# Kernel tuning notes

Measured on AMD Instinct MI355X. Metric: run time of the kernel, lower is better.

The kernel has to match this reference:

```python
import jax, jax.numpy as jnp
import numpy as np
import math

B_SZ, L_SEQ, IN_DIM, D_MODEL, OUT_DIM = 8, 4096, 256, 512, 256
RMIN, RMAX = 0.8, 0.99


def setup_inputs() -> dict:
    key = jax.random.key(0)
    ks = jax.random.split(key, 9)
    inputs = jax.random.normal(ks[0], (B_SZ, L_SEQ, IN_DIM), dtype=jnp.float32)
    # A-parameterization per LRUBlock.init_A
    u1 = jax.random.uniform(ks[1], (D_MODEL,), dtype=jnp.float32)
    u2 = jax.random.uniform(ks[2], (D_MODEL,), dtype=jnp.float32)
    nu_log = jnp.log(-0.5 * jnp.log(u1 * (RMAX + RMIN) * (RMAX - RMIN) + RMIN ** 2))
    theta_log = jnp.log(2 * math.pi * u2)
    # NB: original stores gamma (not log gamma) and exponentiates it in forward; replicate.
    gamma_log = jnp.sqrt(1.0 - jnp.exp(-jnp.exp(nu_log)) ** 2)
    B_re = jax.random.uniform(ks[3], (D_MODEL, IN_DIM), dtype=jnp.float32) / math.sqrt(2 * IN_DIM)
    B_im = jax.random.uniform(ks[4], (D_MODEL, IN_DIM), dtype=jnp.float32) / math.sqrt(2 * IN_DIM)
    C_re = jax.random.uniform(ks[5], (OUT_DIM, D_MODEL), dtype=jnp.float32) / math.sqrt(D_MODEL)
    C_im = jax.random.uniform(ks[6], (OUT_DIM, D_MODEL), dtype=jnp.float32) / math.sqrt(D_MODEL)
    D = jax.random.uniform(ks[7], (OUT_DIM, IN_DIM), dtype=jnp.float32) / math.sqrt(IN_DIM)
    return {"inputs": inputs, "nu_log": nu_log, "theta_log": theta_log,
            "gamma_log": gamma_log, "B_re": B_re, "B_im": B_im,
            "C_re": C_re, "C_im": C_im, "D": D}


def reference(inputs, nu_log, theta_log, gamma_log, B_re, B_im, C_re, C_im, D):
    # skip connection: [b, l, in] x [out, in] -> [b, l, out]
    skip = jnp.einsum('blh,dh->bld', inputs, D)
    L = inputs.shape[1]
    # diagonal complex transition A = exp(-exp(nu) + i*exp(theta)), [d_model]
    A = jnp.exp(jax.lax.complex(-jnp.exp(nu_log), jnp.exp(theta_log)))
    Bc = jax.lax.complex(B_re, B_im) * jnp.exp(gamma_log)[:, None]
    # input projection u = inputs @ B^T : [b, l, d_model] complex64
    u = jnp.einsum('blh,dh->bld', inputs.astype(jnp.complex64), Bc)
    # convolution kernel H[d, t] = A[d]^t, linear conv via length-2L FFT
    H = A[:, None] ** jnp.arange(L)  # [d_model, L]
    n = 2 * L
    h_f = jnp.fft.fft(H, n=n, axis=1)          # [d_model, 2L]
    u_f = jnp.fft.fft(u, n=n, axis=1)          # [b, 2L, d_model]
    x = jnp.fft.ifft(u_f * h_f.T, axis=1)[:, :L]  # [b, L, d_model] complex64
    y = jnp.einsum('blh,nh->bln', x, jax.lax.complex(C_re, C_im)).real + skip
    return (x, y)
```

## Files before the change

kernel.cpp:

```cpp
#include <hip/hip_runtime.h>
#include <math.h>

#define B_SZ 8
#define L_SEQ 4096
#define IN_DIM 256
#define D_MODEL 512
#define OUT_DIM 256
#define M_ROWS (B_SZ*L_SEQ)
#define CH 64
#define NCH (L_SEQ/CH)

#define Y_OFF ((size_t)M_ROWS*D_MODEL)

#define XIM_B   ((size_t)0)
#define WT_B    ((size_t)33554432)
#define CDT_B   ((size_t)34078720)
#define S_B     ((size_t)34734080)

typedef __attribute__((ext_vector_type(8))) short short8;
typedef __attribute__((ext_vector_type(4))) float f32x4;
typedef unsigned short ushort_t;

__device__ __forceinline__ unsigned short f2b(float f) {
    unsigned u = __float_as_uint(f);
    unsigned r = u + 0x7FFF + ((u >> 16) & 1);
    return (unsigned short)(r >> 16);
}
__device__ __forceinline__ float b2f(unsigned short v) {
    return __uint_as_float((unsigned)v << 16);
}

__global__ void build_wt(const float* __restrict__ B_re, const float* __restrict__ B_im,
                         const float* __restrict__ gamma_log, ushort_t* __restrict__ Wt) {
    int idx = blockIdx.x*256 + threadIdx.x;
    int half = idx >> 17;
    int r = idx & 131071;
    int d = r >> 8;
    float eg = expf(gamma_log[d]);
    float v = (half ? B_im[r] : B_re[r]) * eg;
    Wt[(size_t)(half*512 + d)*256 + (r & 255)] = f2b(v);
}

__global__ void build_cdt(const float* __restrict__ C_re, const float* __restrict__ C_im,
                          const float* __restrict__ Dm, ushort_t* __restrict__ CDt) {
    int idx = blockIdx.x*256 + threadIdx.x;
    int n = idx / 1280, k = idx % 1280;
    float v;
    if      (k < 512)  v =  C_re[n*512 + k];
    else if (k < 1024) v = -C_im[n*512 + (k-512)];
    else               v =  Dm[n*256 + (k-1024)];
    CDt[idx] = f2b(v);
}

__global__ __launch_bounds__(256) void gemm_u(const float* __restrict__ inp, const ushort_t* __restrict__ Wt,
                                              float* __restrict__ xre, ushort_t* __restrict__ xim) {
    __shared__ ushort_t Al[128][40];
    __shared__ ushort_t Bl[128][40];
    const int tid = threadIdx.x;
    const int wave = tid >> 6, lane = tid & 63;
    const int wr = wave >> 1, wc = wave & 1;
    const int fr = lane & 15, kg = lane >> 4;
    const int row0 = blockIdx.y*128, col0 = blockIdx.x*128;
    const int sr = tid >> 1, sh = (tid & 1)*16;
    f32x4 acc[4][4] = {};
    for (int k0 = 0; k0 < IN_DIM; k0 += 32) {
        const float* ap = inp + (size_t)(row0+sr)*IN_DIM + k0 + sh;
        float4 a0 = *(const float4*)(ap+0), a1 = *(const float4*)(ap+4);
        float4 a2 = *(const float4*)(ap+8), a3 = *(const float4*)(ap+12);
        const ushort_t* bp = Wt + (size_t)(col0+sr)*IN_DIM + k0 + sh;
        uint4 b0 = *(const uint4*)bp, b1 = *(const uint4*)(bp+8);
        ushort_t av[16];
        av[0]=f2b(a0.x); av[1]=f2b(a0.y); av[2]=f2b(a0.z); av[3]=f2b(a0.w);
        av[4]=f2b(a1.x); av[5]=f2b(a1.y); av[6]=f2b(a1.z); av[7]=f2b(a1.w);
        av[8]=f2b(a2.x); av[9]=f2b(a2.y); av[10]=f2b(a2.z); av[11]=f2b(a2.w);
        av[12]=f2b(a3.x); av[13]=f2b(a3.y); av[14]=f2b(a3.z); av[15]=f2b(a3.w);
        __syncthreads();
        *(uint4*)&Al[sr][sh]   = *(uint4*)&av[0];
        *(uint4*)&Al[sr][sh+8] = *(uint4*)&av[8];
        *(uint4*)&Bl[sr][sh]   = b0;
        *(uint4*)&Bl[sr][sh+8] = b1;
        __syncthreads();
        short8 af[4], bf[4];
        #pragma unroll
        for (int m = 0; m < 4; ++m) af[m] = *(const short8*)&Al[wr*64 + m*16 + fr][kg*8];
        #pragma unroll
        for (int n = 0; n < 4; ++n) bf[n] = *(const short8*)&Bl[wc*64 + n*16 + fr][kg*8];
        #pragma unroll
        for (int m = 0; m < 4; ++m)
            #pragma unroll
            for (int n = 0; n < 4; ++n)
                acc[m][n] = __builtin_amdgcn_mfma_f32_16x16x32_bf16(af[m], bf[n], acc[m][n], 0, 0, 0);
    }
    #pragma unroll
    for (int m = 0; m < 4; ++m)
        #pragma unroll
        for (int n = 0; n < 4; ++n) {
            int col = col0 + wc*64 + n*16 + fr;
            #pragma unroll
            for (int j = 0; j < 4; ++j) {
                int row = row0 + wr*64 + m*16 + kg*4 + j;
                if (col0 < 512) xre[(size_t)row*D_MODEL + col] = acc[m][n][j];
                else            xim[(size_t)row*D_MODEL + col - 512] = f2b(acc[m][n][j]);
            }
        }
}

__global__ __launch_bounds__(256) void gemm_y(const float* __restrict__ xre, const ushort_t* __restrict__ xim,
                                              const float* __restrict__ inp, const ushort_t* __restrict__ CDt,
                                              float* __restrict__ y) {
    __shared__ ushort_t Al[128][40];
    __shared__ ushort_t Bl[128][40];
    const int tid = threadIdx.x;
    const int wave = tid >> 6, lane = tid & 63;
    const int wr = wave >> 1, wc = wave & 1;
    const int fr = lane & 15, kg = lane >> 4;
    const int row0 = blockIdx.y*128, col0 = blockIdx.x*128;
    const int sr = tid >> 1, sh = (tid & 1)*16;
    f32x4 acc[4][4] = {};
    for (int k0 = 0; k0 < 1280; k0 += 32) {
        ushort_t av[16];
        if (k0 < 512) {
            const float* ap = xre + (size_t)(row0+sr)*D_MODEL + k0 + sh;
            #pragma unroll
            for (int i = 0; i < 16; i += 4) {
                float4 f = *(const float4*)(ap + i);
                av[i]=f2b(f.x); av[i+1]=f2b(f.y); av[i+2]=f2b(f.z); av[i+3]=f2b(f.w);
            }
        } else if (k0 < 1024) {
            const ushort_t* ap = xim + (size_t)(row0+sr)*D_MODEL + (k0-512) + sh;
            *(uint4*)&av[0] = *(const uint4*)ap;
            *(uint4*)&av[8] = *(const uint4*)(ap+8);
        } else {
            const float* ap = inp + (size_t)(row0+sr)*IN_DIM + (k0-1024) + sh;
            #pragma unroll
            for (int i = 0; i < 16; i += 4) {
                float4 f = *(const float4*)(ap + i);
                av[i]=f2b(f.x); av[i+1]=f2b(f.y); av[i+2]=f2b(f.z); av[i+3]=f2b(f.w);
            }
        }
        const ushort_t* bp = CDt + (size_t)(col0+sr)*1280 + k0 + sh;
        uint4 b0 = *(const uint4*)bp, b1 = *(const uint4*)(bp+8);
        __syncthreads();
        *(uint4*)&Al[sr][sh]   = *(uint4*)&av[0];
        *(uint4*)&Al[sr][sh+8] = *(uint4*)&av[8];
        *(uint4*)&Bl[sr][sh]   = b0;
        *(uint4*)&Bl[sr][sh+8] = b1;
        __syncthreads();
        short8 af[4], bf[4];
        #pragma unroll
        for (int m = 0; m < 4; ++m) af[m] = *(const short8*)&Al[wr*64 + m*16 + fr][kg*8];
        #pragma unroll
        for (int n = 0; n < 4; ++n) bf[n] = *(const short8*)&Bl[wc*64 + n*16 + fr][kg*8];
        #pragma unroll
        for (int m = 0; m < 4; ++m)
            #pragma unroll
            for (int n = 0; n < 4; ++n)
                acc[m][n] = __builtin_amdgcn_mfma_f32_16x16x32_bf16(af[m], bf[n], acc[m][n], 0, 0, 0);
    }
    #pragma unroll
    for (int m = 0; m < 4; ++m)
        #pragma unroll
        for (int n = 0; n < 4; ++n) {
            int col = col0 + wc*64 + n*16 + fr;
            #pragma unroll
            for (int j = 0; j < 4; ++j) {
                int row = row0 + wr*64 + m*16 + kg*4 + j;
                y[(size_t)row*OUT_DIM + col] = acc[m][n][j];
            }
        }
}

__global__ void scan_phase1(const float* __restrict__ xre, const ushort_t* __restrict__ xim,
                            const float* __restrict__ nu_log, const float* __restrict__ theta_log,
                            float2* __restrict__ s) {
    int idx = blockIdx.x*256 + threadIdx.x;
    int d = idx & (D_MODEL-1);
    int c = (idx >> 9) & (NCH-1);
    int b = idx >> 15;
    float en = expf(nu_log[d]), et = expf(theta_log[d]);
    float mag = expf(-en);
    float ar = mag*cosf(et), ai = mag*sinf(et);
    float hr = 0.f, hi = 0.f;
    size_t off = ((size_t)(b*L_SEQ) + c*CH)*D_MODEL + d;
    #pragma unroll 4
    for (int j = 0; j < CH; ++j) {
        float ur = xre[off], ui = b2f(xim[off]);
        float nr = ar*hr - ai*hi + ur;
        float ni = ar*hi + ai*hr + ui;
        hr = nr; hi = ni;
        off += D_MODEL;
    }
    s[idx] = make_float2(hr, hi);
}

__global__ void scan_phase2(const float* __restrict__ nu_log, const float* __restrict__ theta_log,
                            float2* __restrict__ s) {
    int idx = blockIdx.x*256 + threadIdx.x;
    int d = idx & (D_MODEL-1);
    int b = idx >> 9;
    float en = expf(nu_log[d]), et = expf(theta_log[d]);
    float mag = expf(-(float)CH*en);
    float ang = (float)CH*et;
    float aCr = mag*cosf(ang), aCi = mag*sinf(ang);
    float er = 0.f, ei = 0.f;
    float2* sp = s + (size_t)b*NCH*D_MODEL + d;
    for (int c8 = 0; c8 < NCH; c8 += 8) {
        float2 v[8];
        #pragma unroll
        for (int i = 0; i < 8; ++i) v[i] = sp[(size_t)(c8+i)*D_MODEL];
        #pragma unroll
        for (int i = 0; i < 8; ++i) {
            sp[(size_t)(c8+i)*D_MODEL] = make_float2(er, ei);
            float nr = aCr*er - aCi*ei + v[i].x;
            float ni = aCr*ei + aCi*er + v[i].y;
            er = nr; ei = ni;
        }
    }
}

__global__ void scan_phase3(float* __restrict__ xre, ushort_t* __restrict__ xim,
                            const float* __restrict__ nu_log, const float* __restrict__ theta_log,
                            const float2* __restrict__ s) {
    int idx = blockIdx.x*256 + threadIdx.x;
    int d = idx & (D_MODEL-1);
    int c = (idx >> 9) & (NCH-1);
    int b = idx >> 15;
    float en = expf(nu_log[d]), et = expf(theta_log[d]);
    float mag = expf(-en);
    float ar = mag*cosf(et), ai = mag*sinf(et);
    float2 carry = s[idx];
    float hr = carry.x, hi = carry.y;
    size_t off = ((size_t)(b*L_SEQ) + c*CH)*D_MODEL + d;
    #pragma unroll 4
    for (int j = 0; j < CH; ++j) {
        float ur = xre[off], ui = b2f(xim[off]);
        float nr = ar*hr - ai*hi + ur;
        float ni = ar*hi + ai*hr + ui;
        hr = nr; hi = ni;
        xre[off] = hr; xim[off] = f2b(hi);
        off += D_MODEL;
    }
}

extern "C" void kernel_launch(void* const* d_in, const int* in_sizes, int n_in,
                              void* d_out, int out_size, void* d_ws, size_t ws_size,
                              hipStream_t stream) {
    const float* inp       = (const float*)d_in[0];
    const float* nu_log    = (const float*)d_in[1];
    const float* theta_log = (const float*)d_in[2];
    const float* gamma_log = (const float*)d_in[3];
    const float* B_re      = (const float*)d_in[4];
    const float* B_im      = (const float*)d_in[5];
    const float* C_re      = (const float*)d_in[6];
    const float* C_im      = (const float*)d_in[7];
    const float* Dm        = (const float*)d_in[8];
    float* out = (float*)d_out;
    char* wsb  = (char*)d_ws;
    ushort_t* Xim = (ushort_t*)(wsb + XIM_B);
    ushort_t* Wt  = (ushort_t*)(wsb + WT_B);
    ushort_t* CDt = (ushort_t*)(wsb + CDT_B);
    float2*   S   = (float2*)  (wsb + S_B);

    build_wt<<<1024, 256, 0, stream>>>(B_re, B_im, gamma_log, Wt);
    build_cdt<<<1280, 256, 0, stream>>>(C_re, C_im, Dm, CDt);

    dim3 gu(1024/128, M_ROWS/128);
    gemm_u<<<gu, 256, 0, stream>>>(inp, Wt, out, Xim);

    scan_phase1<<<(B_SZ*NCH*D_MODEL)/256, 256, 0, stream>>>(out, Xim, nu_log, theta_log, S);
    scan_phase2<<<(B_SZ*D_MODEL)/256, 256, 0, stream>>>(nu_log, theta_log, S);
    scan_phase3<<<(B_SZ*NCH*D_MODEL)/256, 256, 0, stream>>>(out, Xim, nu_log, theta_log, S);

    dim3 gy(OUT_DIM/128, M_ROWS/128);
    gemm_y<<<gy, 256, 0, stream>>>(out, Xim, inp, CDt, out + Y_OFF);
}
```

Measured before the change: 287.8 us.

## Interleave u re/im as packed bf16 pairs, swizzle GEMM tiles, pack conversions

The weight matrix is interleaved so gemm_u writes u as adjacent bf16 (re, im) pairs into the fp32 x buffer. The scan phases then read one 32-bit word per element instead of separate fp32 and bf16 arrays, and phase3 overwrites each word in place with the fp32 real state plus a separate bf16 imag store. Both GEMMs add a workgroup-index swizzle meant to improve cache locality, and they use packed float2-to-bf16 conversions. The aim is to cut gemm_u output traffic and scan read traffic, at the cost of storing the u real part in bf16, which lowers precision.

Result: faster. 267.7 us (-7.0%).

```diff
diff --git a/kernel.cpp b/kernel.cpp
--- a/kernel.cpp
+++ b/kernel.cpp
@@ -1,4 +1,5 @@
 #include <hip/hip_runtime.h>
+#include <hip/hip_bf16.h>
 #include <math.h>
 
 #define B_SZ 8
@@ -26,19 +27,22 @@
     unsigned r = u + 0x7FFF + ((u >> 16) & 1);
     return (unsigned short)(r >> 16);
 }
-__device__ __forceinline__ float b2f(unsigned short v) {
-    return __uint_as_float((unsigned)v << 16);
+__device__ __forceinline__ float b2f(unsigned v) {
+    return __uint_as_float(v << 16);
+}
+__device__ __forceinline__ unsigned pk2(float lo, float hi) {
+    __hip_bfloat162 h = __float22bfloat162_rn(make_float2(lo, hi));
+    return *(unsigned*)&h;
 }
 
 __global__ void build_wt(const float* __restrict__ B_re, const float* __restrict__ B_im,
                          const float* __restrict__ gamma_log, ushort_t* __restrict__ Wt) {
     int idx = blockIdx.x*256 + threadIdx.x;
-    int half = idx >> 17;
-    int r = idx & 131071;
-    int d = r >> 8;
+    int r = idx >> 8, h = idx & 255;
+    int d = r >> 1, comp = r & 1;
     float eg = expf(gamma_log[d]);
-    float v = (half ? B_im[r] : B_re[r]) * eg;
-    Wt[(size_t)(half*512 + d)*256 + (r & 255)] = f2b(v);
+    float v = (comp ? B_im[d*256 + h] : B_re[d*256 + h]) * eg;
+    Wt[idx] = f2b(v);
 }
 
 __global__ void build_cdt(const float* __restrict__ C_re, const float* __restrict__ C_im,
@@ -53,14 +57,17 @@
 }
 
 __global__ __launch_bounds__(256) void gemm_u(const float* __restrict__ inp, const ushort_t* __restrict__ Wt,
-                                              float* __restrict__ xre, ushort_t* __restrict__ xim) {
+                                              ushort_t* __restrict__ xpair) {
     __shared__ ushort_t Al[128][40];
     __shared__ ushort_t Bl[128][40];
     const int tid = threadIdx.x;
+    const int nwg = gridDim.x * gridDim.y;
+    int orig = blockIdx.y * gridDim.x + blockIdx.x;
+    int wg = (orig & 7) * (nwg >> 3) + (orig >> 3);
+    const int row0 = (wg / gridDim.x) * 128, col0 = (wg % gridDim.x) * 128;
     const int wave = tid >> 6, lane = tid & 63;
     const int wr = wave >> 1, wc = wave & 1;
     const int fr = lane & 15, kg = lane >> 4;
-    const int row0 = blockIdx.y*128, col0 = blockIdx.x*128;
     const int sr = tid >> 1, sh = (tid & 1)*16;
     f32x4 acc[4][4] = {};
     for (int k0 = 0; k0 < IN_DIM; k0 += 32) {
@@ -69,14 +76,14 @@
         float4 a2 = *(const float4*)(ap+8), a3 = *(const float4*)(ap+12);
         const ushort_t* bp = Wt + (size_t)(col0+sr)*IN_DIM + k0 + sh;
         uint4 b0 = *(const uint4*)bp, b1 = *(const uint4*)(bp+8);
-        ushort_t av[16];
-        av[0]=f2b(a0.x); av[1]=f2b(a0.y); av[2]=f2b(a0.z); av[3]=f2b(a0.w);
-        av[4]=f2b(a1.x); av[5]=f2b(a1.y); av[6]=f2b(a1.z); av[7]=f2b(a1.w);
-        av[8]=f2b(a2.x); av[9]=f2b(a2.y); av[10]=f2b(a2.z); av[11]=f2b(a2.w);
-        av[12]=f2b(a3.x); av[13]=f2b(a3.y); av[14]=f2b(a3.z); av[15]=f2b(a3.w);
+        unsigned av[8];
+        av[0]=pk2(a0.x,a0.y); av[1]=pk2(a0.z,a0.w);
+        av[2]=pk2(a1.x,a1.y); av[3]=pk2(a1.z,a1.w);
+        av[4]=pk2(a2.x,a2.y); av[5]=pk2(a2.z,a2.w);
+        av[6]=pk2(a3.x,a3.y); av[7]=pk2(a3.z,a3.w);
         __syncthreads();
         *(uint4*)&Al[sr][sh]   = *(uint4*)&av[0];
-        *(uint4*)&Al[sr][sh+8] = *(uint4*)&av[8];
+        *(uint4*)&Al[sr][sh+8] = *(uint4*)&av[4];
         *(uint4*)&Bl[sr][sh]   = b0;
         *(uint4*)&Bl[sr][sh+8] = b1;
         __syncthreads();
@@ -99,8 +106,7 @@
             #pragma unroll
             for (int j = 0; j < 4; ++j) {
                 int row = row0 + wr*64 + m*16 + kg*4 + j;
-                if (col0 < 512) xre[(size_t)row*D_MODEL + col] = acc[m][n][j];
-                else            xim[(size_t)row*D_MODEL + col - 512] = f2b(acc[m][n][j]);
+                xpair[(size_t)row*1024 + col] = f2b(acc[m][n][j]);
             }
         }
 }
@@ -111,38 +117,43 @@
     __shared__ ushort_t Al[128][40];
     __shared__ ushort_t Bl[128][40];
     const int tid = threadIdx.x;
+    const int nwg = gridDim.x * gridDim.y;
+    int orig = blockIdx.y * gridDim.x + blockIdx.x;
+    int wg = (orig & 7) * (nwg >> 3) + (orig >> 3);
+    const int row0 = (wg / gridDim.x) * 128, col0 = (wg % gridDim.x) * 128;
     const int wave = tid >> 6, lane = tid & 63;
     const int wr = wave >> 1, wc = wave & 1;
     const int fr = lane & 15, kg = lane >> 4;
-    const int row0 = blockIdx.y*128, col0 = blockIdx.x*128;
     const int sr = tid >> 1, sh = (tid & 1)*16;
     f32x4 acc[4][4] = {};
     for (int k0 = 0; k0 < 1280; k0 += 32) {
-        ushort_t av[16];
+        unsigned av[8];
         if (k0 < 512) {
             const float* ap = xre + (size_t)(row0+sr)*D_MODEL + k0 + sh;
             #pragma unroll
-            for (int i = 0; i < 16; i += 4) {
-                float4 f = *(const float4*)(ap + i);
-                av[i]=f2b(f.x); av[i+1]=f2b(f.y); av[i+2]=f2b(f.z); av[i+3]=f2b(f.w);
+            for (int i = 0; i < 4; ++i) {
+                float4 f = *(const float4*)(ap + i*4);
+                av[2*i]   = pk2(f.x, f.y);
+                av[2*i+1] = pk2(f.z, f.w);
             }
         } else if (k0 < 1024) {
             const ushort_t* ap = xim + (size_t)(row0+sr)*D_MODEL + (k0-512) + sh;
             *(uint4*)&av[0] = *(const uint4*)ap;
-            *(uint4*)&av[8] = *(const uint4*)(ap+8);
+            *(uint4*)&av[4] = *(const uint4*)(ap+8);
         } else {
             const float* ap = inp + (size_t)(row0+sr)*IN_DIM + (k0-1024) + sh;
             #pragma unroll
-            for (int i = 0; i < 16; i += 4) {
-                float4 f = *(const float4*)(ap + i);
-                av[i]=f2b(f.x); av[i+1]=f2b(f.y); av[i+2]=f2b(f.z); av[i+3]=f2b(f.w);
+            for (int i = 0; i < 4; ++i) {
+                float4 f = *(const float4*)(ap + i*4);
+                av[2*i]   = pk2(f.x, f.y);
+                av[2*i+1] = pk2(f.z, f.w);
             }
         }
         const ushort_t* bp = CDt + (size_t)(col0+sr)*1280 + k0 + sh;
         uint4 b0 = *(const uint4*)bp, b1 = *(const uint4*)(bp+8);
         __syncthreads();
         *(uint4*)&Al[sr][sh]   = *(uint4*)&av[0];
-        *(uint4*)&Al[sr][sh+8] = *(uint4*)&av[8];
+        *(uint4*)&Al[sr][sh+8] = *(uint4*)&av[4];
         *(uint4*)&Bl[sr][sh]   = b0;
         *(uint4*)&Bl[sr][sh+8] = b1;
         __syncthreads();
@@ -170,7 +181,7 @@
         }
 }
 
-__global__ void scan_phase1(const float* __restrict__ xre, const ushort_t* __restrict__ xim,
+__global__ void scan_phase1(const unsigned* __restrict__ xp,
                             const float* __restrict__ nu_log, const float* __restrict__ theta_log,
                             float2* __restrict__ s) {
     int idx = blockIdx.x*256 + threadIdx.x;
@@ -184,7 +195,8 @@
     size_t off = ((size_t)(b*L_SEQ) + c*CH)*D_MODEL + d;
     #pragma unroll 4
     for (int j = 0; j < CH; ++j) {
-        float ur = xre[off], ui = b2f(xim[off]);
+        unsigned p = xp[off];
+        float ur = b2f(p & 0xffffu), ui = b2f(p >> 16);
         float nr = ar*hr - ai*hi + ur;
         float ni = ar*hi + ai*hr + ui;
         hr = nr; hi = ni;
@@ -218,7 +230,7 @@
     }
 }
 
-__global__ void scan_phase3(float* __restrict__ xre, ushort_t* __restrict__ xim,
+__global__ void scan_phase3(unsigned* __restrict__ xp, ushort_t* __restrict__ xim,
                             const float* __restrict__ nu_log, const float* __restrict__ theta_log,
                             const float2* __restrict__ s) {
     int idx = blockIdx.x*256 + threadIdx.x;
@@ -233,11 +245,13 @@
     size_t off = ((size_t)(b*L_SEQ) + c*CH)*D_MODEL + d;
     #pragma unroll 4
     for (int j = 0; j < CH; ++j) {
-        float ur = xre[off], ui = b2f(xim[off]);
+        unsigned p = xp[off];
+        float ur = b2f(p & 0xffffu), ui = b2f(p >> 16);
         float nr = ar*hr - ai*hi + ur;
         float ni = ar*hi + ai*hr + ui;
         hr = nr; hi = ni;
-        xre[off] = hr; xim[off] = f2b(hi);
+        xp[off] = __float_as_uint(hr);
+        xim[off] = f2b(hi);
         off += D_MODEL;
     }
 }
@@ -265,11 +279,11 @@
     build_cdt<<<1280, 256, 0, stream>>>(C_re, C_im, Dm, CDt);
 
     dim3 gu(1024/128, M_ROWS/128);
-    gemm_u<<<gu, 256, 0, stream>>>(inp, Wt, out, Xim);
-
-    scan_phase1<<<(B_SZ*NCH*D_MODEL)/256, 256, 0, stream>>>(out, Xim, nu_log, theta_log, S);
+    gemm_u<<<gu, 256, 0, stream>>>(inp, Wt, (ushort_t*)out);
+
+    scan_phase1<<<(B_SZ*NCH*D_MODEL)/256, 256, 0, stream>>>((const unsigned*)out, nu_log, theta_log, S);
     scan_phase2<<<(B_SZ*D_MODEL)/256, 256, 0, stream>>>(nu_log, theta_log, S);
-    scan_phase3<<<(B_SZ*NCH*D_MODEL)/256, 256, 0, stream>>>(out, Xim, nu_log, theta_log, S);
+    scan_phase3<<<(B_SZ*NCH*D_MODEL)/256, 256, 0, stream>>>((unsigned*)out, Xim, nu_log, theta_log, S);
 
     dim3 gy(OUT_DIM/128, M_ROWS/128);
     gemm_y<<<gy, 256, 0, stream>>>(out, Xim, inp, CDt, out + Y_OFF);
```
